# Kernel tuning notes

Measured on AMD Instinct MI355X. Metric: run time of the kernel, lower is better.

Reference implementation:

```python
import jax, jax.numpy as jnp
import numpy as np

NEG = -1e30  # safe -inf surrogate (avoids nan grads through where)
NUM_CLASSES = 128
BLANK = NUM_CLASSES - 1
B, T, L = 256, 512, 64


def setup_inputs() -> dict:
    key = jax.random.key(0)
    k1, k2, k3, k4 = jax.random.split(key, 4)
    y_pred = jax.random.normal(k1, (B, T, NUM_CLASSES), dtype=jnp.float32)
    y_true = jax.random.randint(k2, (B, L), 0, BLANK, dtype=jnp.int32)  # labels in [0, C-2]
    input_length = jax.random.randint(k3, (B,), T // 2, T + 1, dtype=jnp.int32)
    label_length = jax.random.randint(k4, (B,), L // 2, L + 1, dtype=jnp.int32)
    return {"y_true": y_true, "y_pred": y_pred,
            "input_length": input_length, "label_length": label_length}


def ctc_loss(y_pred, y_true, input_length, label_length):
    # y_pred: [B,T,C] logits (batch-major), y_true: [B,L] int labels, blank = C-1.
    Bs, Ts, C = y_pred.shape
    Ls = y_true.shape[1]
    S = 2 * Ls + 1  # extended label lattice: blank, l1, blank, l2, ..., blank
    lp = jax.nn.log_softmax(y_pred.astype(jnp.float32), axis=-1)  # [B,T,C]
    z = jnp.full((Bs, S), BLANK, dtype=jnp.int32).at[:, 1::2].set(y_true)  # [B,S]
    idx = jnp.broadcast_to(z[:, None, :], (Bs, Ts, S))
    lp_z = jnp.take_along_axis(lp, idx, axis=2)  # [B,T,S] log p(z_s | t)
    # skip transition s-2 -> s allowed when z_s is a label differing from z_{s-2}
    s_idx = jnp.arange(S)
    z_m2 = jnp.pad(z[:, :-2], ((0, 0), (2, 0)), constant_values=BLANK)
    skip = (s_idx[None, :] >= 2) & (z != BLANK) & (z != z_m2)  # [B,S]
    alpha0 = (jnp.full((Bs, S), NEG, jnp.float32)
              .at[:, 0].set(lp_z[:, 0, 0])
              .at[:, 1].set(lp_z[:, 0, 1]))
    lps = jnp.moveaxis(lp_z[:, 1:, :], 1, 0)  # [T-1, B, S]
    ts = jnp.arange(1, Ts)

    def step(alpha, xs):
        t, lpt = xs
        a1 = jnp.pad(alpha[:, :-1], ((0, 0), (1, 0)), constant_values=NEG)
        a2 = jnp.where(skip, jnp.pad(alpha[:, :-2], ((0, 0), (2, 0)), constant_values=NEG), NEG)
        new = jnp.logaddexp(jnp.logaddexp(alpha, a1), a2) + lpt
        # freeze rows whose sequence already ended (t >= input_length)
        alpha = jnp.where((t < input_length)[:, None], new, alpha)
        return alpha, None

    alphaT, _ = jax.lax.scan(step, alpha0, (ts, lps))
    e1 = (2 * label_length)[:, None]  # final blank position per row
    a_end = jnp.take_along_axis(alphaT, e1, axis=1)[:, 0]
    a_end2 = jnp.take_along_axis(alphaT, e1 - 1, axis=1)[:, 0]
    return -jnp.logaddexp(a_end, a_end2)  # [B] negative log-likelihood


def reference(y_true, y_pred, input_length, label_length):
    # tf.nn.ctc_loss(labels, logits, label_length, logit_length,
    #                logits_time_major=False, blank_index=num_classes-1)
    return ctc_loss(y_pred, y_true, input_length, label_length)
```

## Files before the change

kernel.cpp:

```cpp
#include <hip/hip_runtime.h>
#include <hip/hip_fp16.h>
#include <math.h>


constexpr int Cc = 128;
constexpr int Tt = 512;
constexpr int Ll = 64;
constexpr int NCk = Tt / 8;
constexpr float INV_LN2 = 1.4426950408889634f;
constexpr float LN2_F   = 0.6931471805599453f;

__device__ __forceinline__ float fexp2(float x) { return __builtin_amdgcn_exp2f(x); }
__device__ __forceinline__ float flog2(float x) { return __builtin_amdgcn_logf(x); }

template<int CTRL, bool BC>
__device__ __forceinline__ float dppf(float old, float x) {
    return __int_as_float(__builtin_amdgcn_update_dpp(
        __float_as_int(old), __float_as_int(x), CTRL, 0xF, 0xF, BC));
}
__device__ __forceinline__ float wshr1(float x, float fill) { return dppf<0x138, false>(fill, x); }

__device__ __forceinline__ float rlf(float v, int lane) {
    return __int_as_float(__builtin_amdgcn_readlane(__float_as_int(v), lane));
}
__device__ __forceinline__ float rowsum(float e) {
    e += dppf<0x111, true>(0.f, e);
    e += dppf<0x112, true>(0.f, e);
    e += dppf<0x114, true>(0.f, e);
    e += dppf<0x118, true>(0.f, e);
    return e;
}
__device__ __forceinline__ float rowmax(float m) {
    m = fmaxf(m, dppf<0x111, true>(0.f, m));
    m = fmaxf(m, dppf<0x112, true>(0.f, m));
    m = fmaxf(m, dppf<0x114, true>(0.f, m));
    m = fmaxf(m, dppf<0x118, true>(0.f, m));
    return m;
}
__device__ __forceinline__ float allmax(float m) {
    m = rowmax(m);
    return fmaxf(fmaxf(rlf(m, 15), rlf(m, 31)), fmaxf(rlf(m, 47), rlf(m, 63)));
}
__device__ __forceinline__ float bperm_f(int srclane, float v) {
    return __int_as_float(__builtin_amdgcn_ds_bpermute(srclane << 2, __float_as_int(v)));
}
__device__ __forceinline__ float gather4(float4 v, int srclane, int csel) {
    const float gx = bperm_f(srclane, v.x), gy = bperm_f(srclane, v.y);
    const float gz = bperm_f(srclane, v.z), gw = bperm_f(srclane, v.w);
    const float lo = (csel & 1) ? gy : gx;
    const float hi = (csel & 1) ? gw : gz;
    return (csel & 2) ? hi : lo;
}

template<bool GUARD>
__device__ __forceinline__ void window4(const float* wv, const float* ws,
                                        int t0, int inlen,
                                        float& aO, float& aE, float& r0,
                                        float& Rtot, float& pendSc, float& pendR)
{
    aO = fminf(aO * pendSc, 1.3e36f);
    aE = fminf(aE * pendSc, 1.3e36f);
    r0 *= pendSc;
    Rtot += pendR;
    const float M = allmax(fmaxf(fmaxf(aO, aE), r0));
    int R = (int)(__float_as_uint(M) >> 23) - 127;
    R = (R < -126) ? -126 : ((R > 126) ? 126 : R);
    pendSc = __uint_as_float((unsigned)(127 - R) << 23);
    pendR = (float)R;
#pragma unroll
    for (int j = 0; j < 4; ++j) {
        if (!GUARD || (t0 + j < inlen)) {
            const float pE = wshr1(aE, r0);
            const float pO = wshr1(aO, 0.0f);
            const float nO = fmaf(aO, wv[j], fmaf(pO, ws[j], pE * wv[j]));
            aE += aO;
            aO = nO;
        }
    }
}

__global__ __launch_bounds__(1024, 1) void ctc_fused3_kernel(
    const int* __restrict__ y_true,
    const float* __restrict__ y_pred,
    const int* __restrict__ in_len,
    const int* __restrict__ lab_len,
    float* __restrict__ out)
{
    __shared__ __half w_lds[Tt / 8][64][8];
    __shared__ float  ps[16];

    const int b   = blockIdx.x;
    const int tid = threadIdx.x;
    const int w   = tid >> 6;
    const int l   = tid & 63;

    int inlen = in_len[b]; if (inlen < 1) inlen = 1; if (inlen > Tt) inlen = Tt;
    int LLv   = lab_len[b]; if (LLv < 1) LLv = 1; if (LLv > Ll) LLv = Ll;

    const int lab = y_true[b * Ll + l] & 127;
    const float* rowbase = y_pred + (size_t)b * Tt * Cc;

    const int half = l >> 5, li = l & 31;
    const int srcA = lab >> 2;
    const int csel = lab & 3;
    const int tbase = w * 32;
    const bool live = (l < LLv);

    float4 vb[4];
#pragma unroll
    for (int j = 0; j < 4; ++j)
        vb[j] = ((const float4*)(rowbase + (size_t)(tbase + 2 * j + half) * Cc))[li];

    float acc = 0.0f;

    for (int i = 0; i < 16; i += 4) {
#pragma unroll
        for (int j = 0; j < 4; ++j) {
            const float4 v = vb[j];
            const int nx = i + 4 + j;
            if (nx < 16)
                vb[j] = ((const float4*)(rowbase + (size_t)(tbase + 2 * nx + half) * Cc))[li];

            const int rA = tbase + 2 * (i + j);
            const int rB = rA + 1;

            float e = (fexp2(v.x * INV_LN2) + fexp2(v.y * INV_LN2))
                    + (fexp2(v.z * INV_LN2) + fexp2(v.w * INV_LN2));
            e = rowsum(e);
            const float sA = rlf(e, 15) + rlf(e, 31);
            const float sB = rlf(e, 47) + rlf(e, 63);
            const float lsA = flog2(sA), lsB = flog2(sB);
            const float blA = rlf(v.w, 31);
            const float blB = rlf(v.w, 63);

            const float lpbA = fmaf(blA, INV_LN2, -lsA);
            const float lpbB = fmaf(blB, INV_LN2, -lsB);
            acc += ((rA < inlen) ? lpbA : 0.0f) + ((rB < inlen) ? lpbB : 0.0f);

            const float xA = gather4(v, srcA, csel);
            const float xB = gather4(v, srcA + 32, csel);
            float wA = fminf(fmaxf(fexp2((xA - blA) * INV_LN2), 6.1e-5f), 8192.0f);
            float wB = fminf(fmaxf(fexp2((xB - blB) * INV_LN2), 6.1e-5f), 8192.0f);
            wA = live ? wA : 0.0f;
            wB = live ? wB : 0.0f;
            const unsigned packed =
                  (unsigned)__half_as_ushort(__float2half(wA))
                | ((unsigned)__half_as_ushort(__float2half(wB)) << 16);
            *(unsigned*)&w_lds[rA >> 3][l][rA & 7] = packed;
        }
    }
    if (l == 0) ps[w] = acc;

    __syncthreads();
    if (w != 0) return;

    const int labp = __shfl_up(lab, 1, 64);
    const float skf = ((l >= 1) && (lab != labp)) ? 1.0f : 0.0f;

    float aO = 0.0f, aE = 0.0f, r0 = 1.0f;
    float Rtot = 0.0f, pendSc = 1.0f, pendR = 0.0f;

    const int nchunks = (inlen + 7) >> 3;
    uint4 A = *(const uint4*)&w_lds[0][l][0];
    for (int c = 0; c < nchunks; ++c) {
        const int nx = (c + 1 < NCk) ? c + 1 : NCk - 1;
        const uint4 Bv = *(const uint4*)&w_lds[nx][l][0];

        float wv[8], ws[8];
        {
            const __half2 h0 = *reinterpret_cast<const __half2*>(&A.x);
            const __half2 h1 = *reinterpret_cast<const __half2*>(&A.y);
            const __half2 h2 = *reinterpret_cast<const __half2*>(&A.z);
            const __half2 h3 = *reinterpret_cast<const __half2*>(&A.w);
            wv[0] = __low2float(h0); wv[1] = __high2float(h0);
            wv[2] = __low2float(h1); wv[3] = __high2float(h1);
            wv[4] = __low2float(h2); wv[5] = __high2float(h2);
            wv[6] = __low2float(h3); wv[7] = __high2float(h3);
        }
#pragma unroll
        for (int j = 0; j < 8; ++j) ws[j] = skf * wv[j];

        const int t0 = c * 8;
        if (t0 + 8 <= inlen) {
            window4<false>(wv,     ws,     t0,     inlen, aO, aE, r0, Rtot, pendSc, pendR);
            window4<false>(wv + 4, ws + 4, t0 + 4, inlen, aO, aE, r0, Rtot, pendSc, pendR);
        } else {
            window4<true >(wv,     ws,     t0,     inlen, aO, aE, r0, Rtot, pendSc, pendR);
            window4<true >(wv + 4, ws + 4, t0 + 4, inlen, aO, aE, r0, Rtot, pendSc, pendR);
        }
        A = Bv;
    }

    float cum_b = 0.0f;
#pragma unroll
    for (int q = 0; q < 16; ++q) cum_b += ps[q];

    const float aEr = __shfl(aE, LLv - 1, 64);
    const float aOr = __shfl(aO, LLv - 1, 64);
    if (l == 0)
        out[b] = -LN2_F * (flog2(fmaxf(aEr + aOr, 1e-37f)) + Rtot + cum_b);
}

extern "C" void kernel_launch(void* const* d_in, const int* in_sizes, int n_in,
                              void* d_out, int out_size, void* d_ws, size_t ws_size,
                              hipStream_t stream) {
    const int*   y_true  = (const int*)d_in[0];
    const float* y_pred  = (const float*)d_in[1];
    const int*   in_len  = (const int*)d_in[2];
    const int*   lab_len = (const int*)d_in[3];
    float*       out     = (float*)d_out;
    (void)d_ws; (void)ws_size;

    ctc_fused3_kernel<<<256, 1024, 0, stream>>>(y_true, y_pred, in_len, lab_len, out);
}
```

Baseline: 122.3 us.

## Run CTC alpha recurrence in fp64 with rescaling every 32 steps

Moves the serial alpha recursion from fp32 to fp64 so the larger exponent range lets the wave-wide max renormalization run once every 4 chunks instead of every 4 time steps. The per-step float scale/clamp and the reduction feeding it are removed from the critical path. In exchange, each step now needs two DPP shifts per shifted value plus fp64 add and multiply, which MI355X runs at lower throughput and with a longer dependent latency than fp32. The final log is computed from a manually split exponent and mantissa.

```diff
diff --git a/kernel.cpp b/kernel.cpp
--- a/kernel.cpp
+++ b/kernel.cpp
@@ -14,14 +14,25 @@
 __device__ __forceinline__ float flog2(float x) { return __builtin_amdgcn_logf(x); }
 
 template<int CTRL, bool BC>
+__device__ __forceinline__ int dppi(int old, int x) {
+    return __builtin_amdgcn_update_dpp(old, x, CTRL, 0xF, 0xF, BC);
+}
+template<int CTRL, bool BC>
 __device__ __forceinline__ float dppf(float old, float x) {
-    return __int_as_float(__builtin_amdgcn_update_dpp(
-        __float_as_int(old), __float_as_int(x), CTRL, 0xF, 0xF, BC));
+    return __int_as_float(dppi<CTRL, BC>(__float_as_int(old), __float_as_int(x)));
 }
 __device__ __forceinline__ float wshr1(float x, float fill) { return dppf<0x138, false>(fill, x); }
+__device__ __forceinline__ double wshr1_d(double x, double fill) {
+    const int rl = dppi<0x138, false>(__double2loint(fill), __double2loint(x));
+    const int rh = dppi<0x138, false>(__double2hiint(fill), __double2hiint(x));
+    return __hiloint2double(rh, rl);
+}
 
 __device__ __forceinline__ float rlf(float v, int lane) {
     return __int_as_float(__builtin_amdgcn_readlane(__float_as_int(v), lane));
+}
+__device__ __forceinline__ unsigned rlu(unsigned v, int lane) {
+    return (unsigned)__builtin_amdgcn_readlane((int)v, lane);
 }
 __device__ __forceinline__ float rowsum(float e) {
     e += dppf<0x111, true>(0.f, e);
@@ -30,16 +41,17 @@
     e += dppf<0x118, true>(0.f, e);
     return e;
 }
-__device__ __forceinline__ float rowmax(float m) {
-    m = fmaxf(m, dppf<0x111, true>(0.f, m));
-    m = fmaxf(m, dppf<0x112, true>(0.f, m));
-    m = fmaxf(m, dppf<0x114, true>(0.f, m));
-    m = fmaxf(m, dppf<0x118, true>(0.f, m));
+__device__ __forceinline__ unsigned umaxu(unsigned a, unsigned b) { return a > b ? a : b; }
+__device__ __forceinline__ unsigned rowmax_u(unsigned m) {
+    m = umaxu(m, (unsigned)dppi<0x111, true>(0, (int)m));
+    m = umaxu(m, (unsigned)dppi<0x112, true>(0, (int)m));
+    m = umaxu(m, (unsigned)dppi<0x114, true>(0, (int)m));
+    m = umaxu(m, (unsigned)dppi<0x118, true>(0, (int)m));
     return m;
 }
-__device__ __forceinline__ float allmax(float m) {
-    m = rowmax(m);
-    return fmaxf(fmaxf(rlf(m, 15), rlf(m, 31)), fmaxf(rlf(m, 47), rlf(m, 63)));
+__device__ __forceinline__ unsigned allmax_u(unsigned m) {
+    m = rowmax_u(m);
+    return umaxu(umaxu(rlu(m, 15), rlu(m, 31)), umaxu(rlu(m, 47), rlu(m, 63)));
 }
 __device__ __forceinline__ float bperm_f(int srclane, float v) {
     return __int_as_float(__builtin_amdgcn_ds_bpermute(srclane << 2, __float_as_int(v)));
@@ -52,34 +64,7 @@
     return (csel & 2) ? hi : lo;
 }
 
-template<bool GUARD>
-__device__ __forceinline__ void window4(const float* wv, const float* ws,
-                                        int t0, int inlen,
-                                        float& aO, float& aE, float& r0,
-                                        float& Rtot, float& pendSc, float& pendR)
-{
-    aO = fminf(aO * pendSc, 1.3e36f);
-    aE = fminf(aE * pendSc, 1.3e36f);
-    r0 *= pendSc;
-    Rtot += pendR;
-    const float M = allmax(fmaxf(fmaxf(aO, aE), r0));
-    int R = (int)(__float_as_uint(M) >> 23) - 127;
-    R = (R < -126) ? -126 : ((R > 126) ? 126 : R);
-    pendSc = __uint_as_float((unsigned)(127 - R) << 23);
-    pendR = (float)R;
-#pragma unroll
-    for (int j = 0; j < 4; ++j) {
-        if (!GUARD || (t0 + j < inlen)) {
-            const float pE = wshr1(aE, r0);
-            const float pO = wshr1(aO, 0.0f);
-            const float nO = fmaf(aO, wv[j], fmaf(pO, ws[j], pE * wv[j]));
-            aE += aO;
-            aO = nO;
-        }
-    }
-}
-
-__global__ __launch_bounds__(1024, 1) void ctc_fused3_kernel(
+__global__ __launch_bounds__(1024, 1) void ctc_fused4_kernel(
     const int* __restrict__ y_true,
     const float* __restrict__ y_pred,
     const int* __restrict__ in_len,
@@ -155,10 +140,10 @@
     if (w != 0) return;
 
     const int labp = __shfl_up(lab, 1, 64);
-    const float skf = ((l >= 1) && (lab != labp)) ? 1.0f : 0.0f;
-
-    float aO = 0.0f, aE = 0.0f, r0 = 1.0f;
-    float Rtot = 0.0f, pendSc = 1.0f, pendR = 0.0f;
+    const bool skb = (l >= 1) && (lab != labp);
+
+    double aO = 0.0, aE = 0.0, r0 = 1.0;
+    float Rtot = 0.0f;
 
     const int nchunks = (inlen + 7) >> 3;
     uint4 A = *(const uint4*)&w_lds[0][l][0];
@@ -166,39 +151,73 @@
         const int nx = (c + 1 < NCk) ? c + 1 : NCk - 1;
         const uint4 Bv = *(const uint4*)&w_lds[nx][l][0];
 
-        float wv[8], ws[8];
+        double wd[8];
         {
             const __half2 h0 = *reinterpret_cast<const __half2*>(&A.x);
             const __half2 h1 = *reinterpret_cast<const __half2*>(&A.y);
             const __half2 h2 = *reinterpret_cast<const __half2*>(&A.z);
             const __half2 h3 = *reinterpret_cast<const __half2*>(&A.w);
-            wv[0] = __low2float(h0); wv[1] = __high2float(h0);
-            wv[2] = __low2float(h1); wv[3] = __high2float(h1);
-            wv[4] = __low2float(h2); wv[5] = __high2float(h2);
-            wv[6] = __low2float(h3); wv[7] = __high2float(h3);
-        }
-#pragma unroll
-        for (int j = 0; j < 8; ++j) ws[j] = skf * wv[j];
+            wd[0] = (double)__low2float(h0); wd[1] = (double)__high2float(h0);
+            wd[2] = (double)__low2float(h1); wd[3] = (double)__high2float(h1);
+            wd[4] = (double)__low2float(h2); wd[5] = (double)__high2float(h2);
+            wd[6] = (double)__low2float(h3); wd[7] = (double)__high2float(h3);
+        }
 
         const int t0 = c * 8;
         if (t0 + 8 <= inlen) {
-            window4<false>(wv,     ws,     t0,     inlen, aO, aE, r0, Rtot, pendSc, pendR);
-            window4<false>(wv + 4, ws + 4, t0 + 4, inlen, aO, aE, r0, Rtot, pendSc, pendR);
+#pragma unroll
+            for (int j = 0; j < 8; ++j) {
+                const double pE = wshr1_d(aE, r0);
+                const double pO = wshr1_d(aO, 0.0);
+                const double pOs = skb ? pO : 0.0;
+                const double nO = (aO + pE + pOs) * wd[j];
+                aE += aO;
+                aO = nO;
+            }
         } else {
-            window4<true >(wv,     ws,     t0,     inlen, aO, aE, r0, Rtot, pendSc, pendR);
-            window4<true >(wv + 4, ws + 4, t0 + 4, inlen, aO, aE, r0, Rtot, pendSc, pendR);
+#pragma unroll
+            for (int j = 0; j < 8; ++j) {
+                if (t0 + j < inlen) {
+                    const double pE = wshr1_d(aE, r0);
+                    const double pO = wshr1_d(aO, 0.0);
+                    const double pOs = skb ? pO : 0.0;
+                    const double nO = (aO + pE + pOs) * wd[j];
+                    aE += aO;
+                    aO = nO;
+                }
+            }
         }
         A = Bv;
+
+        if ((c & 3) == 3) {
+            unsigned m = umaxu(umaxu((unsigned)__double2hiint(aE),
+                                     (unsigned)__double2hiint(aO)),
+                               (unsigned)__double2hiint(r0));
+            const unsigned M = allmax_u(m);
+            int R = (int)(M >> 20) - 1023;
+            R = (R < -1020) ? -1020 : ((R > 1020) ? 1020 : R);
+            const double sc = __hiloint2double((1023 - R) << 20, 0);
+            aO *= sc; aE *= sc; r0 *= sc;
+            Rtot += (float)R;
+        }
     }
 
     float cum_b = 0.0f;
 #pragma unroll
     for (int q = 0; q < 16; ++q) cum_b += ps[q];
 
-    const float aEr = __shfl(aE, LLv - 1, 64);
-    const float aOr = __shfl(aO, LLv - 1, 64);
-    if (l == 0)
-        out[b] = -LN2_F * (flog2(fmaxf(aEr + aOr, 1e-37f)) + Rtot + cum_b);
+    const double aEr = __shfl(aE, LLv - 1, 64);
+    const double aOr = __shfl(aO, LLv - 1, 64);
+    if (l == 0) {
+        double v = aEr + aOr;
+        if (!(v > 0.0)) v = 1e-300;
+        const int hi = __double2hiint(v);
+        const int e2 = ((hi >> 20) & 0x7ff) - 1023;
+        const double mant = __hiloint2double((hi & 0x000FFFFF) | (1023 << 20),
+                                             __double2loint(v));
+        const float lg = flog2((float)mant) + (float)e2;
+        out[b] = -LN2_F * (lg + Rtot + cum_b);
+    }
 }
 
 extern "C" void kernel_launch(void* const* d_in, const int* in_sizes, int n_in,
@@ -211,5 +230,5 @@
     float*       out     = (float*)d_out;
     (void)d_ws; (void)ws_size;
 
-    ctc_fused3_kernel<<<256, 1024, 0, stream>>>(y_true, y_pred, in_len, lab_len, out);
-}
+    ctc_fused4_kernel<<<256, 1024, 0, stream>>>(y_true, y_pred, in_len, lab_len, out);
+}
```

Result: no change. 121.1 us (-1.0%).
